# Kernel optimization log

Hardware: AMD Instinct MI355X
Metric: run time of the kernel (lower is better)

## Reference

```python
import jax, jax.numpy as jnp
import numpy as np

B, N, M = 64, 256, 16
ONF, OEF = 92, 41
NF, EF = 128, 64
FINAL = 128  # final_node_len; final_layer outputs FINAL//2


def _linear_params(key, fan_in, fan_out):
    # kaiming_uniform fan_in, relu: bound = sqrt(6/fan_in)
    bound = np.sqrt(6.0 / fan_in)
    W = jax.random.uniform(key, (fan_out, fan_in), jnp.float32, -bound, bound)
    b = jnp.zeros((fan_out,), jnp.float32)
    return W, b


def setup_inputs() -> dict:
    key = jax.random.key(0)
    ks = jax.random.split(key, 12)
    node_fea = jax.random.normal(ks[0], (B, N, ONF), jnp.float32)
    edge_fea = jax.random.normal(ks[1], (B, N, M, OEF), jnp.float32)
    edge_fea_idx = jax.random.randint(ks[2], (B, N, M), 0, N)
    dis = jax.random.uniform(ks[3], (N, N), jnp.float32)
    Wn, bn = _linear_params(ks[4], ONF, NF)
    We, be = _linear_params(ks[5], OEF, EF)
    W1, b1 = _linear_params(ks[6], 2 * NF + EF, 2 * NF)
    W2, b2 = _linear_params(ks[7], 2 * NF + EF, 2 * NF)
    W3, b3 = _linear_params(ks[8], 2 * NF + EF, 2 * NF)
    Wf, bf = _linear_params(ks[9], NF, FINAL // 2)
    return dict(node_fea=node_fea, edge_fea=edge_fea, edge_fea_idx=edge_fea_idx,
                dis=dis, Wn=Wn, bn=bn, We=We, be=be,
                W1=W1, b1=b1, a1=jnp.float32(0.7),
                W2=W2, b2=b2, a2=jnp.float32(0.7),
                W3=W3, b3=b3, a3=jnp.float32(0.7),
                Wf=Wf, bf=bf,
                DAw=jnp.float32(48.0 / 5.0), DAb=jnp.float32(-28.0 / 5.0))


def _conv(nf, ef, idx, W, b, alpha):
    # nf: [B,N,F]; ef: [B,N,M,E]; idx: [B,N,M]
    Bb, Nn, Mm = idx.shape
    F = nf.shape[-1]
    idx_c = jnp.maximum(idx, 0)
    gathered = jax.vmap(lambda x, i: x[i])(nf, idx_c)           # [B,N,M,F]
    self_exp = jnp.broadcast_to(nf[:, :, None, :], (Bb, Nn, Mm, F))
    total = jnp.concatenate([self_exp, gathered, ef], axis=-1)   # [B,N,M,2F+E]
    gated = jnp.einsum('bnmi,oi->bnmo', total, W) + b            # [B,N,M,2F]
    nbr_filter, nbr_core = jnp.split(gated, 2, axis=-1)
    mask = (idx >= 0).astype(nf.dtype)[..., None]
    nbr_filter = jax.nn.sigmoid(nbr_filter) * mask
    nbr_core = jax.nn.softplus(nbr_core)
    nbr_sumed = jnp.sum(nbr_filter * nbr_core, axis=2)           # [B,N,F]
    return jax.nn.softplus(alpha * nf + nbr_sumed)


def reference(node_fea, edge_fea, edge_fea_idx, dis,
              Wn, bn, We, be,
              W1, b1, a1, W2, b2, a2, W3, b3, a3,
              Wf, bf, DAw, DAb):
    nf = node_fea @ Wn.T + bn                                    # [B,N,NF]
    ef = edge_fea @ We.T + be                                    # [B,N,M,EF]
    nf = _conv(nf, ef, edge_fea_idx, W1, b1, a1)
    nf = _conv(nf, ef, edge_fea_idx, W2, b2, a2)
    nf = _conv(nf, ef, edge_fea_idx, W3, b3, a3)
    nf = nf @ Wf.T + bf                                          # [B,N,FINAL//2]
    DA = jax.nn.sigmoid(DAw * dis + DAb)                         # [N,N]
    node1 = jnp.einsum('ij,bjf->bif', DA, nf)
    return jnp.concatenate([nf, node1], axis=2)                  # [B,N,FINAL]
```

## Files before the change

### kernel.cpp

```cpp
#include <hip/hip_runtime.h>
#include <hip/hip_bf16.h>
#include <math.h>

#define Bb   64
#define Nn   256
#define Mm   16
#define ONF  92
#define OEF  41
#define NF   128
#define EF   64
#define KDIM 320
#define ODIM 256
#define FINAL 128
#define K0C  6
#define GRP  4
#define NODESB (4*GRP)

#define LOG2E_F 1.44269504088896f
#define LN2_F   0.6931471805599453f

typedef __attribute__((ext_vector_type(8))) short short8;
typedef __attribute__((ext_vector_type(4))) float f32x4;

#define AS1 __attribute__((address_space(1)))
#define AS3 __attribute__((address_space(3)))

__device__ __forceinline__ void gl2lds16(const void* gp, void* lp) {
    __builtin_amdgcn_global_load_lds((AS1 void*)(void*)gp, (AS3 void*)lp, 16, 0, 0);
}
#define KEEP8(x) asm volatile("" : "+v"(x))

__device__ __forceinline__ float sigmoidf_(float x) {
    float e = __expf(-x);
    return __builtin_amdgcn_rcpf(1.0f + e);
}
__device__ __forceinline__ float softplusf_(float x) {
    return fmaxf(x, 0.0f) + __logf(1.0f + __expf(-fabsf(x)));
}
__device__ __forceinline__ __hip_bfloat16 to_bf16(float x) { return __float2bfloat16(x); }

__device__ __forceinline__ void swz(const float* __restrict__ in, __hip_bfloat16* __restrict__ out,
                                    int t, int Itot, int koff, int Kuse, int K0, float scale)
{
    int j = t & 7;
    int u = t >> 3;
    int lane = u & 63;
    int ln16 = lane & 15, q = lane >> 4;
    int v = u >> 6;
    int k0 = v % K0, tile = v / K0;
    int n = tile * 16 + ln16, k = k0 * 32 + q * 8 + j;
    out[t] = (k < Kuse) ? to_bf16(scale * in[(size_t)n * Itot + koff + k]) : to_bf16(0.0f);
}

#define SZ_WET (OEF * EF)
#define SZ_WB  (16 * K0C * 512)
#define SZ_WS  (16 * 4 * 512)
#define SZ_WNB ((NF / 16) * 3 * 512)
#define SZ_WEB ((EF / 16) * 2 * 512)
#define SZ_WFB ((64 / 16) * 4 * 512)
#define SZ_DA  (Nn * Nn)
#define PREP_TOTAL (SZ_WET + 3 * SZ_WB + 3 * SZ_WS + SZ_WNB + SZ_WEB + SZ_WFB + SZ_DA)

__global__ __launch_bounds__(256) void k_prep(
    const float* __restrict__ We, const float* __restrict__ W1,
    const float* __restrict__ W2, const float* __restrict__ W3,
    const float* __restrict__ Wn, const float* __restrict__ Wf,
    const float* __restrict__ dis, const float* __restrict__ pw, const float* __restrict__ pb,
    float* __restrict__ WeT,
    __hip_bfloat16* __restrict__ W1b, __hip_bfloat16* __restrict__ W2b, __hip_bfloat16* __restrict__ W3b,
    __hip_bfloat16* __restrict__ W1s, __hip_bfloat16* __restrict__ W2s, __hip_bfloat16* __restrict__ W3s,
    __hip_bfloat16* __restrict__ Wnb, __hip_bfloat16* __restrict__ Web, __hip_bfloat16* __restrict__ Wfb,
    __hip_bfloat16* __restrict__ DAf)
{
    int t = blockIdx.x * 256 + threadIdx.x;
    if (t < SZ_WET) {
        int o = t / OEF, i = t - o * OEF;
        WeT[i * EF + o] = We[t];
        return;
    }
    t -= SZ_WET;
    if (t < SZ_WB) { swz(W1, W1b, t, KDIM, NF, 192, K0C, LOG2E_F); return; }
    t -= SZ_WB;
    if (t < SZ_WB) { swz(W2, W2b, t, KDIM, NF, 192, K0C, LOG2E_F); return; }
    t -= SZ_WB;
    if (t < SZ_WB) { swz(W3, W3b, t, KDIM, NF, 192, K0C, LOG2E_F); return; }
    t -= SZ_WB;
    if (t < SZ_WS) { swz(W1, W1s, t, KDIM, 0, NF, 4, LOG2E_F); return; }
    t -= SZ_WS;
    if (t < SZ_WS) { swz(W2, W2s, t, KDIM, 0, NF, 4, LOG2E_F); return; }
    t -= SZ_WS;
    if (t < SZ_WS) { swz(W3, W3s, t, KDIM, 0, NF, 4, LOG2E_F); return; }
    t -= SZ_WS;
    if (t < SZ_WNB) { swz(Wn, Wnb, t, ONF, 0, ONF, 3, 1.0f); return; }
    t -= SZ_WNB;
    if (t < SZ_WEB) { swz(We, Web, t, OEF, 0, OEF, 2, 1.0f); return; }
    t -= SZ_WEB;
    if (t < SZ_WFB) { swz(Wf, Wfb, t, NF, 0, NF, 4, 1.0f); return; }
    t -= SZ_WFB;
    if (t < SZ_DA) {
        int i = t >> 8, jx = t & 255;
        float v = sigmoidf_(fmaf(*pw, dis[t], *pb));
        int itile = i >> 4, ln16 = i & 15;
        int k0 = jx >> 5, q = (jx >> 3) & 3, jj = jx & 7;
        DAf[(size_t)((((itile * 8 + k0) << 6) + (q << 4) + ln16)) * 8 + jj] = to_bf16(v);
    }
}

template<int KIN, int K0, int NCOLS>
__device__ __forceinline__ void emb_body(
    int bid, const float* __restrict__ X, const __hip_bfloat16* __restrict__ Bswz,
    const float* __restrict__ bias, __hip_bfloat16* __restrict__ Y,
    __hip_bfloat16* A_s, __hip_bfloat16* O_s)
{
    constexpr int KP = K0 * 32;
    constexpr int TPW = NCOLS / 64;
    constexpr int OLD = NCOLS + 24;

    const int row0 = bid * 64;
    const int t = threadIdx.x;

    {
        const float4* Xb = (const float4*)(X + (size_t)row0 * KIN);
        constexpr int NV = (64 * KIN) / 4;
        for (int c = t; c < NV; c += 256) {
            float4 v = Xb[c];
            int flat = c * 4;
            #pragma unroll
            for (int e = 0; e < 4; e++) {
                int f = flat + e;
                int row = f / KIN, k = f - row * KIN;
                int mt = row >> 4, ln16 = row & 15;
                int k0 = k >> 5, q = (k >> 3) & 3, j = k & 7;
                float vv = (e == 0) ? v.x : (e == 1) ? v.y : (e == 2) ? v.z : v.w;
                A_s[(((mt * K0 + k0) << 6) + (q << 4) + ln16) * 8 + j] = to_bf16(vv);
            }
        }
        constexpr int PAD = KP - KIN;
        for (int c = t; c < 64 * PAD; c += 256) {
            int row = c / PAD, k = KIN + (c - row * PAD);
            int mt = row >> 4, ln16 = row & 15;
            int k0 = k >> 5, q = (k >> 3) & 3, j = k & 7;
            A_s[(((mt * K0 + k0) << 6) + (q << 4) + ln16) * 8 + j] = to_bf16(0.0f);
        }
    }
    __syncthreads();

    const int wv = t >> 6, lane = t & 63;
    const int q = lane >> 4, ln16 = lane & 15;

    f32x4 acc[4][TPW];
    #pragma unroll
    for (int p = 0; p < TPW; p++) {
        float bv = bias[(wv * TPW + p) * 16 + ln16];
        #pragma unroll
        for (int mt = 0; mt < 4; mt++) acc[mt][p] = (f32x4){bv, bv, bv, bv};
    }

    short8 bw[TPW][K0];
    #pragma unroll
    for (int p = 0; p < TPW; p++)
        #pragma unroll
        for (int k0 = 0; k0 < K0; k0++)
            bw[p][k0] = *(const short8*)(Bswz + ((size_t)((wv * TPW + p) * K0 + k0) << 9) + (lane << 3));

    #pragma unroll
    for (int k0 = 0; k0 < K0; k0++) {
        short8 af[4];
        #pragma unroll
        for (int mt = 0; mt < 4; mt++)
            af[mt] = *(const short8*)(A_s + (((mt * K0 + k0) << 6) + lane) * 8);
        #pragma unroll
        for (int mt = 0; mt < 4; mt++)
            #pragma unroll
            for (int p = 0; p < TPW; p++)
                acc[mt][p] = __builtin_amdgcn_mfma_f32_16x16x32_bf16(af[mt], bw[p][k0], acc[mt][p], 0, 0, 0);
    }

    #pragma unroll
    for (int mt = 0; mt < 4; mt++)
        #pragma unroll
        for (int p = 0; p < TPW; p++) {
            int col = (wv * TPW + p) * 16 + ln16;
            #pragma unroll
            for (int r = 0; r < 4; r++)
                O_s[(mt * 16 + q * 4 + r) * OLD + col] = to_bf16(acc[mt][p][r]);
        }
    __syncthreads();
    constexpr int CH = NCOLS / 8;
    for (int c = t; c < 64 * CH; c += 256) {
        int row = c / CH, ch = c - row * CH;
        *(uint4*)(Y + (size_t)(row0 + row) * NCOLS + ch * 8) =
            *(const uint4*)(O_s + row * OLD + ch * 8);
    }
}

__global__ __launch_bounds__(256) void k_embed_all(
    const float* __restrict__ node_fea, const __hip_bfloat16* __restrict__ Wnb,
    const float* __restrict__ bn, __hip_bfloat16* __restrict__ nf0,
    const float* __restrict__ edge_fea, const __hip_bfloat16* __restrict__ Web,
    const float* __restrict__ be, __hip_bfloat16* __restrict__ efb)
{
    __shared__ __align__(16) __hip_bfloat16 A_s[4 * 3 * 512];
    __shared__ __align__(16) __hip_bfloat16 O_s[64 * (NF + 24)];
    if (blockIdx.x < 256)
        emb_body<ONF, 3, NF>(blockIdx.x, node_fea, Wnb, bn, nf0, A_s, O_s);
    else
        emb_body<OEF, 2, EF>(blockIdx.x - 256, edge_fea, Web, be, efb, A_s, O_s);
}

__global__ __launch_bounds__(256, 3) void k_conv_blk(
    const __hip_bfloat16* __restrict__ nf_in,
    const __hip_bfloat16* __restrict__ ef_bf,
    const int*   __restrict__ eidx,
    const __hip_bfloat16* __restrict__ Wb,
    const __hip_bfloat16* __restrict__ Wsb,
    const float* __restrict__ bias,
    const float* __restrict__ palpha,
    __hip_bfloat16* __restrict__ nf_out)
{
    __shared__ __align__(16) __hip_bfloat16 A_s[2][4 * K0C * 512];

    const int node0_blk = blockIdx.x * NODESB;
    const int bbase = node0_blk & ~255;
    const int t = threadIdx.x;
    const int wv = t >> 6, lane = t & 63;
    const int q = lane >> 4, ln16 = lane & 15;
    const int row = (wv << 4) + ln16;
    const float alpha = *palpha;

    auto stage_group = [&](int node0g, __hip_bfloat16* buf) -> unsigned long long {
        int mi = eidx[node0g * Mm + row];
        unsigned long long mb = __ballot(eidx[node0g * Mm + lane] >= 0);
        int j = mi < 0 ? 0 : mi;
        const __hip_bfloat16* gathp = nf_in + (size_t)(bbase + j) * NF + q * 8;
        #pragma unroll
        for (int k0 = 0; k0 < 4; k0++)
            gl2lds16(gathp + k0 * 32, buf + (wv * K0C + k0) * 512 + lane * 8);
        const __hip_bfloat16* efp = ef_bf + (size_t)((node0g << 4) + row) * EF + q * 8;
        #pragma unroll
        for (int k0 = 0; k0 < 2; k0++)
            gl2lds16(efp + k0 * 32, buf + (wv * K0C + 4 + k0) * 512 + lane * 8);
        return mb;
    };

    unsigned long long mb_next = stage_group(node0_blk, A_s[0]);

    const __hip_bfloat16* WF0 = Wb + ((size_t)(2 * wv) * (K0C * 512)) + (lane << 3);
    const __hip_bfloat16* WF1 = WF0 + K0C * 512;
    const __hip_bfloat16* WC0 = WF0 + 8 * (K0C * 512);
    const __hip_bfloat16* WC1 = WC0 + K0C * 512;
    short8 mF0[K0C], mF1[K0C], mC0[K0C], mC1[K0C];
    #pragma unroll
    for (int k0 = 0; k0 < K0C; k0++) {
        mF0[k0] = *(const short8*)(WF0 + k0 * 512);
        mF1[k0] = *(const short8*)(WF1 + k0 * 512);
        mC0[k0] = *(const short8*)(WC0 + k0 * 512);
        mC1[k0] = *(const short8*)(WC1 + k0 * 512);
    }

    f32x4 sv[4];
    #pragma unroll
    for (int c = 0; c < 4; c++) {
        int tile = 2 * wv + (c & 1) + ((c >> 1) << 3);
        float bv = bias[tile * 16 + ln16] * LOG2E_F;
        sv[c] = (f32x4){bv, bv, bv, bv};
    }
    #pragma unroll
    for (int k0 = 0; k0 < 4; k0++) {
        short8 afs = *(const short8*)(nf_in + (size_t)(node0_blk + ln16) * NF + k0 * 32 + q * 8);
        #pragma unroll
        for (int c = 0; c < 4; c++) {
            int tile = 2 * wv + (c & 1) + ((c >> 1) << 3);
            short8 bws = *(const short8*)(Wsb + ((size_t)(tile * 4 + k0) << 9) + (lane << 3));
            sv[c] = __builtin_amdgcn_mfma_f32_16x16x32_bf16(afs, bws, sv[c], 0, 0, 0);
        }
    }

    #pragma unroll
    for (int k0 = 0; k0 < K0C; k0++) {
        KEEP8(mF0[k0]); KEEP8(mF1[k0]); KEEP8(mC0[k0]); KEEP8(mC1[k0]);
    }

    __syncthreads();

    int cur = 0;
    for (int g = 0; g < GRP; g++) {
        const int node0g = node0_blk + g * 4;
        const unsigned long long mb_cur = mb_next;
        if (g + 1 < GRP) mb_next = stage_group(node0g + 4, A_s[cur ^ 1]);

        float selfv[8];
        #pragma unroll
        for (int mt = 0; mt < 4; mt++)
            #pragma unroll
            for (int p = 0; p < 2; p++)
                selfv[mt * 2 + p] =
                    __bfloat162float(nf_in[(size_t)(node0g + mt) * NF + (2 * wv + p) * 16 + ln16]);

        const int srcl = (g << 4) + ln16;
        const __hip_bfloat16* Acur = A_s[cur];

        #pragma unroll
        for (int h = 0; h < 2; h++) {
            f32x4 accF[2][2], accC[2][2];
            #pragma unroll
            for (int mtl = 0; mtl < 2; mtl++) {
                const int mt = 2 * h + mtl;
                #pragma unroll
                for (int p = 0; p < 2; p++) {
                    float vF = __shfl(sv[p][mt], srcl);
                    float vC = __shfl(sv[2 + p][mt], srcl);
                    accF[mtl][p] = (f32x4){vF, vF, vF, vF};
                    accC[mtl][p] = (f32x4){vC, vC, vC, vC};
                }
            }
            #pragma unroll
            for (int k0 = 0; k0 < K0C; k0++) {
                short8 af[2];
                #pragma unroll
                for (int mtl = 0; mtl < 2; mtl++)
                    af[mtl] = *(const short8*)(Acur + (((2 * h + mtl) * K0C + k0) * 64 + lane) * 8);
                #pragma unroll
                for (int mtl = 0; mtl < 2; mtl++) {
                    accF[mtl][0] = __builtin_amdgcn_mfma_f32_16x16x32_bf16(af[mtl], mF0[k0], accF[mtl][0], 0, 0, 0);
                    accF[mtl][1] = __builtin_amdgcn_mfma_f32_16x16x32_bf16(af[mtl], mF1[k0], accF[mtl][1], 0, 0, 0);
                    accC[mtl][0] = __builtin_amdgcn_mfma_f32_16x16x32_bf16(af[mtl], mC0[k0], accC[mtl][0], 0, 0, 0);
                    accC[mtl][1] = __builtin_amdgcn_mfma_f32_16x16x32_bf16(af[mtl], mC1[k0], accC[mtl][1], 0, 0, 0);
                }
            }
            #pragma unroll
            for (int mtl = 0; mtl < 2; mtl++) {
                const int mt = 2 * h + mtl;
                const int gnode = node0g + mt;
                unsigned mbits = (unsigned)(mb_cur >> (mt * 16 + q * 4)) & 0xFu;
                #pragma unroll
                for (int p = 0; p < 2; p++) {
                    float partial = 0.0f;
                    #pragma unroll
                    for (int r = 0; r < 4; r++) {
                        bool msk = (mbits >> r) & 1u;
                        float f2 = accF[mtl][p][r];
                        float c2 = accC[mtl][p][r];
                        float sig = __builtin_amdgcn_rcpf(1.0f + __builtin_amdgcn_exp2f(-f2));
                        float sp2 = fmaxf(c2, 0.0f) +
                                    __builtin_amdgcn_logf(1.0f + __builtin_amdgcn_exp2f(-fabsf(c2)));
                        partial += msk ? sig * sp2 : 0.0f;
                    }
                    partial += __shfl_xor(partial, 16);
                    partial += __shfl_xor(partial, 32);
                    if (q == 0) {
                        int col = (2 * wv + p) * 16 + ln16;
                        nf_out[(size_t)gnode * NF + col] =
                            to_bf16(softplusf_(fmaf(alpha, selfv[mt * 2 + p], LN2_F * partial)));
                    }
                }
            }
        }
        __syncthreads();
        cur ^= 1;
    }
}

template<bool PRECOMP>
__global__ __launch_bounds__(256, 3) void k_conv_mfma(
    const __hip_bfloat16* __restrict__ nf_in,
    const float* __restrict__ edge_fea,
    const __hip_bfloat16* __restrict__ ef_bf,
    const int*   __restrict__ eidx,
    const float* __restrict__ WeT,
    const float* __restrict__ be,
    const __hip_bfloat16* __restrict__ Wb,
    const __hip_bfloat16* __restrict__ Wsb,
    const float* __restrict__ bias,
    const float* __restrict__ palpha,
    __hip_bfloat16* __restrict__ nf_out)
{
    __shared__ __align__(16) __hip_bfloat16 A_s[4 * K0C * 512];
    __shared__ __align__(16) __hip_bfloat16 A_sf[4 * 512];

    const int node0 = blockIdx.x * 4;
    const int b = node0 >> 8;
    const int t = threadIdx.x;
    const int wv = t >> 6, lane = t & 63;
    const int q = lane >> 4, ln16 = lane & 15;
    const int row = (wv << 4) + ln16;

    const int myidx = eidx[node0 * Mm + row];
    const unsigned long long mball = __ballot(eidx[node0 * Mm + lane] >= 0);

    float selfv[8];
    #pragma unroll
    for (int mt = 0; mt < 4; mt++)
        #pragma unroll
        for (int p = 0; p < 2; p++)
            selfv[mt * 2 + p] =
                __bfloat162float(nf_in[(size_t)(node0 + mt) * NF + (2 * wv + p) * 16 + ln16]);

    {
        int j = myidx < 0 ? 0 : myidx;
        const __hip_bfloat16* gathp = nf_in + (size_t)((b << 8) + j) * NF;
        #pragma unroll
        for (int k0 = 0; k0 < 4; k0++)
            *(uint4*)(A_s + ((wv * K0C + k0) * 64 + lane) * 8) =
                *(const uint4*)(gathp + k0 * 32 + q * 8);
        *(uint4*)(A_sf + (wv * 64 + lane) * 8) =
            *(const uint4*)(nf_in + (size_t)(node0 + (ln16 & 3)) * NF + wv * 32 + q * 8);
        if (PRECOMP) {
            const __hip_bfloat16* efp = ef_bf + (size_t)((node0 << 4) + row) * EF;
            #pragma unroll
            for (int k0 = 0; k0 < 2; k0++)
                *(uint4*)(A_s + ((wv * K0C + 4 + k0) * 64 + lane) * 8) =
                    *(const uint4*)(efp + k0 * 32 + q * 8);
        } else {
            for (int c = t; c < 64 * EF; c += 256) {
                int rr = c >> 6, col = c & 63;
                float a = be[col];
                const float* er = edge_fea + (size_t)(node0 * Mm + rr) * OEF;
                #pragma unroll
                for (int i = 0; i < OEF; i++) a = fmaf(er[i], WeT[i * EF + col], a);
                int mt = rr >> 4, l16 = rr & 15;
                int k0 = 4 + (col >> 5), qq = (col >> 3) & 3, jj = col & 7;
                A_s[((mt * K0C + k0) * 64 + qq * 16 + l16) * 8 + jj] = to_bf16(a);
            }
        }
    }
    __syncthreads();

    f32x4 sv[4];
    #pragma unroll
    for (int c = 0; c < 4; c++) {
        int tile = 2 * wv + (c & 1) + ((c >> 1) << 3);
        float bv = bias[tile * 16 + ln16] * LOG2E_F;
        sv[c] = (f32x4){bv, bv, bv, bv};
    }
    #pragma unroll
    for (int k0 = 0; k0 < 4; k0++) {
        short8 afs = *(const short8*)(A_sf + (k0 * 64 + lane) * 8);
        #pragma unroll
        for (int c = 0; c < 4; c++) {
            int tile = 2 * wv + (c & 1) + ((c >> 1) << 3);
            short8 bws = *(const short8*)(Wsb + ((size_t)(tile * 4 + k0) << 9) + (lane << 3));
            sv[c] = __builtin_amdgcn_mfma_f32_16x16x32_bf16(afs, bws, sv[c], 0, 0, 0);
        }
    }

    f32x4 accF[4][2], accC[4][2];
    #pragma unroll
    for (int mt = 0; mt < 4; mt++) {
        #pragma unroll
        for (int p = 0; p < 2; p++) {
            float vF = __shfl(sv[p][mt], ln16);
            float vC = __shfl(sv[2 + p][mt], ln16);
            accF[mt][p] = (f32x4){vF, vF, vF, vF};
            accC[mt][p] = (f32x4){vC, vC, vC, vC};
        }
    }

    const __hip_bfloat16* WF0 = Wb + ((size_t)(2 * wv) * (K0C * 512)) + (lane << 3);
    const __hip_bfloat16* WF1 = WF0 + K0C * 512;
    const __hip_bfloat16* WC0 = WF0 + 8 * (K0C * 512);
    const __hip_bfloat16* WC1 = WC0 + K0C * 512;

    #pragma unroll
    for (int k0 = 0; k0 < K0C; k0++) {
        short8 cF0 = *(const short8*)(WF0 + k0 * 512);
        short8 cF1 = *(const short8*)(WF1 + k0 * 512);
        short8 cC0 = *(const short8*)(WC0 + k0 * 512);
        short8 cC1 = *(const short8*)(WC1 + k0 * 512);
        short8 af[4];
        #pragma unroll
        for (int mt = 0; mt < 4; mt++)
            af[mt] = *(const short8*)(A_s + ((mt * K0C + k0) * 64 + lane) * 8);
        #pragma unroll
        for (int mt = 0; mt < 4; mt++) {
            accF[mt][0] = __builtin_amdgcn_mfma_f32_16x16x32_bf16(af[mt], cF0, accF[mt][0], 0, 0, 0);
            accF[mt][1] = __builtin_amdgcn_mfma_f32_16x16x32_bf16(af[mt], cF1, accF[mt][1], 0, 0, 0);
            accC[mt][0] = __builtin_amdgcn_mfma_f32_16x16x32_bf16(af[mt], cC0, accC[mt][0], 0, 0, 0);
            accC[mt][1] = __builtin_amdgcn_mfma_f32_16x16x32_bf16(af[mt], cC1, accC[mt][1], 0, 0, 0);
        }
    }

    const float alpha = *palpha;
    #pragma unroll
    for (int mt = 0; mt < 4; mt++) {
        const int gnode = node0 + mt;
        unsigned mbits = (unsigned)(mball >> (mt * 16 + q * 4)) & 0xFu;
        #pragma unroll
        for (int p = 0; p < 2; p++) {
            float partial = 0.0f;
            #pragma unroll
            for (int r = 0; r < 4; r++) {
                bool msk = (mbits >> r) & 1u;
                float f2 = accF[mt][p][r];
                float c2 = accC[mt][p][r];
                float sig = __builtin_amdgcn_rcpf(1.0f + __builtin_amdgcn_exp2f(-f2));
                float sp2 = fmaxf(c2, 0.0f) +
                            __builtin_amdgcn_logf(1.0f + __builtin_amdgcn_exp2f(-fabsf(c2)));
                partial += msk ? sig * sp2 : 0.0f;
            }
            partial += __shfl_xor(partial, 16);
            partial += __shfl_xor(partial, 32);
            if (q == 0) {
                int col = (2 * wv + p) * 16 + ln16;
                nf_out[(size_t)gnode * NF + col] =
                    to_bf16(softplusf_(fmaf(alpha, selfv[mt * 2 + p], LN2_F * partial)));
            }
        }
    }
}

__global__ __launch_bounds__(256) void k_final_mfma(
    const __hip_bfloat16* __restrict__ nf, const __hip_bfloat16* __restrict__ Wfb,
    const float* __restrict__ bfv, float* __restrict__ out,
    __hip_bfloat16* __restrict__ XT)
{
    __shared__ __align__(16) __hip_bfloat16 A_s[16 * 512];
    const int node0 = blockIdx.x * 64;
    const int bloc = node0 >> 8;
    const int t = threadIdx.x;
    const int wv = t >> 6, lane = t & 63;
    const int q = lane >> 4, ln16 = lane & 15;

    const __hip_bfloat16* rowp = nf + (size_t)(node0 + (wv << 4) + ln16) * NF;
    #pragma unroll
    for (int k0 = 0; k0 < 4; k0++)
        *(uint4*)(A_s + ((wv * 4 + k0) * 64 + lane) * 8) =
            *(const uint4*)(rowp + k0 * 32 + q * 8);
    __syncthreads();

    short8 bw[4];
    #pragma unroll
    for (int k0 = 0; k0 < 4; k0++)
        bw[k0] = *(const short8*)(Wfb + ((size_t)(wv * 4 + k0) * 64 + lane) * 8);

    float bv = bfv[wv * 16 + ln16];
    f32x4 acc[4];
    #pragma unroll
    for (int mt = 0; mt < 4; mt++) acc[mt] = (f32x4){bv, bv, bv, bv};

    #pragma unroll
    for (int k0 = 0; k0 < 4; k0++) {
        short8 af[4];
        #pragma unroll
        for (int mt = 0; mt < 4; mt++)
            af[mt] = *(const short8*)(A_s + ((mt * 4 + k0) * 64 + lane) * 8);
        #pragma unroll
        for (int mt = 0; mt < 4; mt++)
            acc[mt] = __builtin_amdgcn_mfma_f32_16x16x32_bf16(af[mt], bw[k0], acc[mt], 0, 0, 0);
    }

    const int col = (wv << 4) + ln16;
    #pragma unroll
    for (int mt = 0; mt < 4; mt++)
        #pragma unroll
        for (int r = 0; r < 4; r++) {
            int row = mt * 16 + q * 4 + r;
            float v = acc[mt][r];
            out[(size_t)(node0 + row) * FINAL + col] = v;
            XT[(size_t)(bloc * 64 + col) * 256 + (node0 & 255) + row] = to_bf16(v);
        }
}

__global__ __launch_bounds__(256) void k_node1_mfma(
    const __hip_bfloat16* __restrict__ DAf,
    const __hip_bfloat16* __restrict__ XT,
    float* __restrict__ out)
{
    __shared__ __align__(16) __hip_bfloat16 B_s[32 * 512];
    const int blk = blockIdx.x;
    const int b = blk >> 2, i0 = (blk & 3) * 64;
    const int t = threadIdx.x;
    const int wv = t >> 6, lane = t & 63;
    const int q = lane >> 4, ln16 = lane & 15;

    const __hip_bfloat16* xrow = XT + (size_t)(b * 64 + (wv << 4) + ln16) * 256;
    #pragma unroll
    for (int k0 = 0; k0 < 8; k0++)
        *(uint4*)(B_s + ((wv * 8 + k0) * 64 + lane) * 8) =
            *(const uint4*)(xrow + k0 * 32 + q * 8);
    __syncthreads();

    f32x4 acc[4];
    #pragma unroll
    for (int mt = 0; mt < 4; mt++) acc[mt] = (f32x4){0.f, 0.f, 0.f, 0.f};

    #pragma unroll
    for (int k0 = 0; k0 < 8; k0++) {
        short8 bfr = *(const short8*)(B_s + ((wv * 8 + k0) * 64 + lane) * 8);
        short8 af[4];
        #pragma unroll
        for (int mt = 0; mt < 4; mt++)
            af[mt] = *(const short8*)(DAf + (size_t)(((i0 >> 4) + mt) * 8 + k0) * 512 + (lane << 3));
        #pragma unroll
        for (int mt = 0; mt < 4; mt++)
            acc[mt] = __builtin_amdgcn_mfma_f32_16x16x32_bf16(af[mt], bfr, acc[mt], 0, 0, 0);
    }

    #pragma unroll
    for (int mt = 0; mt < 4; mt++)
        #pragma unroll
        for (int r = 0; r < 4; r++) {
            int i = i0 + mt * 16 + q * 4 + r;
            out[(size_t)((b << 8) + i) * FINAL + 64 + (wv << 4) + ln16] = acc[mt][r];
        }
}

extern "C" void kernel_launch(void* const* d_in, const int* in_sizes, int n_in,
                              void* d_out, int out_size, void* d_ws, size_t ws_size,
                              hipStream_t stream)
{
    const float* node_fea = (const float*)d_in[0];
    const float* edge_fea = (const float*)d_in[1];
    const int*   eidx     = (const int*)  d_in[2];
    const float* dis      = (const float*)d_in[3];
    const float* Wn = (const float*)d_in[4];
    const float* bn = (const float*)d_in[5];
    const float* We = (const float*)d_in[6];
    const float* be = (const float*)d_in[7];
    const float* W1 = (const float*)d_in[8];
    const float* b1 = (const float*)d_in[9];
    const float* a1 = (const float*)d_in[10];
    const float* W2 = (const float*)d_in[11];
    const float* b2 = (const float*)d_in[12];
    const float* a2 = (const float*)d_in[13];
    const float* W3 = (const float*)d_in[14];
    const float* b3 = (const float*)d_in[15];
    const float* a3 = (const float*)d_in[16];
    const float* Wf = (const float*)d_in[17];
    const float* bf = (const float*)d_in[18];
    const float* DAw = (const float*)d_in[19];
    const float* DAb = (const float*)d_in[20];
    float* out = (float*)d_out;

    char* base = (char*)d_ws;
    size_t off = 0;
    auto alloc = [&](size_t bytes) { char* p = base + off; off = (off + bytes + 255) & ~(size_t)255; return p; };
    __hip_bfloat16* nfA = (__hip_bfloat16*)alloc((size_t)Bb * Nn * NF * 2);
    __hip_bfloat16* nfB = (__hip_bfloat16*)alloc((size_t)Bb * Nn * NF * 2);
    __hip_bfloat16* W1b = (__hip_bfloat16*)alloc((size_t)SZ_WB * 2);
    __hip_bfloat16* W2b = (__hip_bfloat16*)alloc((size_t)SZ_WB * 2);
    __hip_bfloat16* W3b = (__hip_bfloat16*)alloc((size_t)SZ_WB * 2);
    __hip_bfloat16* W1s = (__hip_bfloat16*)alloc((size_t)SZ_WS * 2);
    __hip_bfloat16* W2s = (__hip_bfloat16*)alloc((size_t)SZ_WS * 2);
    __hip_bfloat16* W3s = (__hip_bfloat16*)alloc((size_t)SZ_WS * 2);
    float* WeT = (float*)alloc((size_t)OEF * EF * 4);
    __hip_bfloat16* DAf = (__hip_bfloat16*)alloc((size_t)Nn * Nn * 2);
    __hip_bfloat16* Wnb = (__hip_bfloat16*)alloc((size_t)SZ_WNB * 2);
    __hip_bfloat16* Web = (__hip_bfloat16*)alloc((size_t)SZ_WEB * 2);
    __hip_bfloat16* Wfb = (__hip_bfloat16*)alloc((size_t)SZ_WFB * 2);
    __hip_bfloat16* XT  = (__hip_bfloat16*)alloc((size_t)Bb * 64 * Nn * 2);
    __hip_bfloat16* efb = (__hip_bfloat16*)alloc((size_t)Bb * Nn * Mm * EF * 2);
    const bool precomp = (ws_size >= off);

    hipLaunchKernelGGL(k_prep, dim3((PREP_TOTAL + 255) / 256), dim3(256), 0, stream,
                       We, W1, W2, W3, Wn, Wf, dis, DAw, DAb,
                       WeT, W1b, W2b, W3b, W1s, W2s, W3s, Wnb, Web, Wfb, DAf);

    hipLaunchKernelGGL(k_embed_all, dim3(precomp ? (256 + Bb * Nn * Mm / 64) : 256), dim3(256), 0, stream,
                       node_fea, Wnb, bn, nfA, edge_fea, Web, be, efb);

    if (precomp) {
        hipLaunchKernelGGL(k_conv_blk, dim3(Bb * Nn / NODESB), dim3(256), 0, stream,
                           nfA, efb, eidx, W1b, W1s, b1, a1, nfB);
        hipLaunchKernelGGL(k_conv_blk, dim3(Bb * Nn / NODESB), dim3(256), 0, stream,
                           nfB, efb, eidx, W2b, W2s, b2, a2, nfA);
        hipLaunchKernelGGL(k_conv_blk, dim3(Bb * Nn / NODESB), dim3(256), 0, stream,
                           nfA, efb, eidx, W3b, W3s, b3, a3, nfB);
    } else {
        hipLaunchKernelGGL((k_conv_mfma<false>), dim3(Bb * Nn / 4), dim3(256), 0, stream,
                           nfA, edge_fea, efb, eidx, WeT, be, W1b, W1s, b1, a1, nfB);
        hipLaunchKernelGGL((k_conv_mfma<false>), dim3(Bb * Nn / 4), dim3(256), 0, stream,
                           nfB, edge_fea, efb, eidx, WeT, be, W2b, W2s, b2, a2, nfA);
        hipLaunchKernelGGL((k_conv_mfma<false>), dim3(Bb * Nn / 4), dim3(256), 0, stream,
                           nfA, edge_fea, efb, eidx, WeT, be, W3b, W3s, b3, a3, nfB);
    }

    hipLaunchKernelGGL(k_final_mfma, dim3(Bb * Nn / 64), dim3(256), 0, stream, nfB, Wfb, bf, out, XT);
    hipLaunchKernelGGL(k_node1_mfma, dim3(Bb * 4), dim3(256), 0, stream, DAf, XT, out);
}
```

Before: 316.8 us.

## Split self-term GEMM into separate kernel and make conv kernel persistent

The per-node self-feature projection (nf times the self slice of W plus bias) moves out of the conv kernel into a standalone MFMA GEMM kernel that writes a float32 S buffer. The conv kernel becomes persistent with a fixed grid of 768 blocks, grid-striding over 4-node groups with double-buffered LDS staging of neighbour and edge tiles. It reads the precomputed S row for each node. This amortises the register-resident weight loads across more groups and removes the per-block self-GEMM and shuffles. In exchange it adds three extra launches and a 16 MB float32 round trip through memory per layer.

```diff
diff --git a/kernel.cpp b/kernel.cpp
--- a/kernel.cpp
+++ b/kernel.cpp
@@ -13,8 +13,8 @@
 #define ODIM 256
 #define FINAL 128
 #define K0C  6
-#define GRP  4
-#define NODESB (4*GRP)
+#define NGRP  (Bb * Nn / 4)
+#define GRIDP 768
 
 #define LOG2E_F 1.44269504088896f
 #define LN2_F   0.6931471805599453f
@@ -208,27 +208,83 @@
         emb_body<OEF, 2, EF>(blockIdx.x - 256, edge_fea, Web, be, efb, A_s, O_s);
 }
 
-__global__ __launch_bounds__(256, 3) void k_conv_blk(
+__global__ __launch_bounds__(256) void k_gemm_s(
+    const __hip_bfloat16* __restrict__ nf,
+    const __hip_bfloat16* __restrict__ Ws,
+    const float* __restrict__ bias,
+    float* __restrict__ S)
+{
+    __shared__ __align__(16) __hip_bfloat16 A_s[16 * 512];
+    const int row0 = blockIdx.x * 64;
+    const int t = threadIdx.x;
+    const int wv = t >> 6, lane = t & 63;
+    const int q = lane >> 4, ln16 = lane & 15;
+
+    #pragma unroll
+    for (int k0 = 0; k0 < 4; k0++)
+        gl2lds16(nf + (size_t)(row0 + (wv << 4) + ln16) * NF + k0 * 32 + q * 8,
+                 A_s + ((wv * 4 + k0) * 64 + lane) * 8);
+    __syncthreads();
+
+    short8 bw[4][4];
+    #pragma unroll
+    for (int p = 0; p < 4; p++)
+        #pragma unroll
+        for (int k0 = 0; k0 < 4; k0++)
+            bw[p][k0] = *(const short8*)(Ws + ((size_t)((wv * 4 + p) * 4 + k0) << 9) + (lane << 3));
+
+    f32x4 acc[4][4];
+    #pragma unroll
+    for (int p = 0; p < 4; p++) {
+        float bv = bias[(wv * 4 + p) * 16 + ln16] * LOG2E_F;
+        #pragma unroll
+        for (int mt = 0; mt < 4; mt++) acc[mt][p] = (f32x4){bv, bv, bv, bv};
+    }
+
+    #pragma unroll
+    for (int k0 = 0; k0 < 4; k0++) {
+        short8 af[4];
+        #pragma unroll
+        for (int mt = 0; mt < 4; mt++)
+            af[mt] = *(const short8*)(A_s + ((mt * 4 + k0) * 64 + lane) * 8);
+        #pragma unroll
+        for (int mt = 0; mt < 4; mt++)
+            #pragma unroll
+            for (int p = 0; p < 4; p++)
+                acc[mt][p] = __builtin_amdgcn_mfma_f32_16x16x32_bf16(af[mt], bw[p][k0], acc[mt][p], 0, 0, 0);
+    }
+
+    #pragma unroll
+    for (int mt = 0; mt < 4; mt++)
+        #pragma unroll
+        for (int p = 0; p < 4; p++) {
+            int col = (wv * 4 + p) * 16 + ln16;
+            #pragma unroll
+            for (int r = 0; r < 4; r++)
+                S[(size_t)(row0 + mt * 16 + q * 4 + r) * ODIM + col] = acc[mt][p][r];
+        }
+}
+
+__global__ __launch_bounds__(256, 3) void k_conv_ps(
     const __hip_bfloat16* __restrict__ nf_in,
     const __hip_bfloat16* __restrict__ ef_bf,
     const int*   __restrict__ eidx,
     const __hip_bfloat16* __restrict__ Wb,
-    const __hip_bfloat16* __restrict__ Wsb,
-    const float* __restrict__ bias,
+    const float* __restrict__ Sbuf,
     const float* __restrict__ palpha,
     __hip_bfloat16* __restrict__ nf_out)
 {
     __shared__ __align__(16) __hip_bfloat16 A_s[2][4 * K0C * 512];
 
-    const int node0_blk = blockIdx.x * NODESB;
-    const int bbase = node0_blk & ~255;
     const int t = threadIdx.x;
     const int wv = t >> 6, lane = t & 63;
     const int q = lane >> 4, ln16 = lane & 15;
     const int row = (wv << 4) + ln16;
     const float alpha = *palpha;
 
-    auto stage_group = [&](int node0g, __hip_bfloat16* buf) -> unsigned long long {
+    auto stage_group = [&](int gi, __hip_bfloat16* buf) -> unsigned long long {
+        const int node0g = gi * 4;
+        const int bbase = node0g & ~255;
         int mi = eidx[node0g * Mm + row];
         unsigned long long mb = __ballot(eidx[node0g * Mm + lane] >= 0);
         int j = mi < 0 ? 0 : mi;
@@ -242,8 +298,6 @@
             gl2lds16(efp + k0 * 32, buf + (wv * K0C + 4 + k0) * 512 + lane * 8);
         return mb;
     };
-
-    unsigned long long mb_next = stage_group(node0_blk, A_s[0]);
 
     const __hip_bfloat16* WF0 = Wb + ((size_t)(2 * wv) * (K0C * 512)) + (lane << 3);
     const __hip_bfloat16* WF1 = WF0 + K0C * 512;
@@ -258,105 +312,70 @@
         mC1[k0] = *(const short8*)(WC1 + k0 * 512);
     }
 
-    f32x4 sv[4];
-    #pragma unroll
-    for (int c = 0; c < 4; c++) {
-        int tile = 2 * wv + (c & 1) + ((c >> 1) << 3);
-        float bv = bias[tile * 16 + ln16] * LOG2E_F;
-        sv[c] = (f32x4){bv, bv, bv, bv};
-    }
-    #pragma unroll
-    for (int k0 = 0; k0 < 4; k0++) {
-        short8 afs = *(const short8*)(nf_in + (size_t)(node0_blk + ln16) * NF + k0 * 32 + q * 8);
-        #pragma unroll
-        for (int c = 0; c < 4; c++) {
-            int tile = 2 * wv + (c & 1) + ((c >> 1) << 3);
-            short8 bws = *(const short8*)(Wsb + ((size_t)(tile * 4 + k0) << 9) + (lane << 3));
-            sv[c] = __builtin_amdgcn_mfma_f32_16x16x32_bf16(afs, bws, sv[c], 0, 0, 0);
-        }
-    }
-
-    #pragma unroll
-    for (int k0 = 0; k0 < K0C; k0++) {
-        KEEP8(mF0[k0]); KEEP8(mF1[k0]); KEEP8(mC0[k0]); KEEP8(mC1[k0]);
-    }
-
-    __syncthreads();
-
+    int g = blockIdx.x;
+    unsigned long long mb_pending = stage_group(g, A_s[0]);
     int cur = 0;
-    for (int g = 0; g < GRP; g++) {
-        const int node0g = node0_blk + g * 4;
-        const unsigned long long mb_cur = mb_next;
-        if (g + 1 < GRP) mb_next = stage_group(node0g + 4, A_s[cur ^ 1]);
-
-        float selfv[8];
-        #pragma unroll
-        for (int mt = 0; mt < 4; mt++)
-            #pragma unroll
-            for (int p = 0; p < 2; p++)
-                selfv[mt * 2 + p] =
-                    __bfloat162float(nf_in[(size_t)(node0g + mt) * NF + (2 * wv + p) * 16 + ln16]);
-
-        const int srcl = (g << 4) + ln16;
+
+    for (; g < NGRP; g += GRIDP) {
+        __syncthreads();
+
+        const unsigned long long mb_now = mb_pending;
+        if (g + GRIDP < NGRP) mb_pending = stage_group(g + GRIDP, A_s[cur ^ 1]);
+
+        #pragma unroll
+        for (int k0 = 0; k0 < K0C; k0++) {
+            KEEP8(mF0[k0]); KEEP8(mF1[k0]); KEEP8(mC0[k0]); KEEP8(mC1[k0]);
+        }
+
+        const int node0g = g * 4;
         const __hip_bfloat16* Acur = A_s[cur];
 
         #pragma unroll
-        for (int h = 0; h < 2; h++) {
-            f32x4 accF[2][2], accC[2][2];
-            #pragma unroll
-            for (int mtl = 0; mtl < 2; mtl++) {
-                const int mt = 2 * h + mtl;
+        for (int mt = 0; mt < 4; mt++) {
+            const int gnode = node0g + mt;
+            const float* Srow = Sbuf + (size_t)gnode * ODIM;
+            f32x4 accF[2], accC[2];
+            float selfv[2];
+            #pragma unroll
+            for (int p = 0; p < 2; p++) {
+                int col = (2 * wv + p) * 16 + ln16;
+                float vF = Srow[col];
+                float vC = Srow[128 + col];
+                accF[p] = (f32x4){vF, vF, vF, vF};
+                accC[p] = (f32x4){vC, vC, vC, vC};
+                selfv[p] = __bfloat162float(nf_in[(size_t)gnode * NF + col]);
+            }
+            #pragma unroll
+            for (int k0 = 0; k0 < K0C; k0++) {
+                short8 af = *(const short8*)(Acur + ((mt * K0C + k0) * 64 + lane) * 8);
+                accF[0] = __builtin_amdgcn_mfma_f32_16x16x32_bf16(af, mF0[k0], accF[0], 0, 0, 0);
+                accF[1] = __builtin_amdgcn_mfma_f32_16x16x32_bf16(af, mF1[k0], accF[1], 0, 0, 0);
+                accC[0] = __builtin_amdgcn_mfma_f32_16x16x32_bf16(af, mC0[k0], accC[0], 0, 0, 0);
+                accC[1] = __builtin_amdgcn_mfma_f32_16x16x32_bf16(af, mC1[k0], accC[1], 0, 0, 0);
+            }
+            unsigned mbits = (unsigned)(mb_now >> (mt * 16 + q * 4)) & 0xFu;
+            #pragma unroll
+            for (int p = 0; p < 2; p++) {
+                float partial = 0.0f;
                 #pragma unroll
-                for (int p = 0; p < 2; p++) {
-                    float vF = __shfl(sv[p][mt], srcl);
-                    float vC = __shfl(sv[2 + p][mt], srcl);
-                    accF[mtl][p] = (f32x4){vF, vF, vF, vF};
-                    accC[mtl][p] = (f32x4){vC, vC, vC, vC};
+                for (int r = 0; r < 4; r++) {
+                    bool msk = (mbits >> r) & 1u;
+                    float f2 = accF[p][r];
+                    float c2 = accC[p][r];
+                    float sig = __builtin_amdgcn_rcpf(1.0f + __builtin_amdgcn_exp2f(-f2));
+                    float sp2 = fmaxf(c2, 0.0f) +
+                                __builtin_amdgcn_logf(1.0f + __builtin_amdgcn_exp2f(-fabsf(c2)));
+                    partial += msk ? sig * sp2 : 0.0f;
+                }
+                partial += __shfl_xor(partial, 16);
+                partial += __shfl_xor(partial, 32);
+                if (q == 0) {
+                    int col = (2 * wv + p) * 16 + ln16;
+                    nf_out[(size_t)gnode * NF + col] =
+                        to_bf16(softplusf_(fmaf(alpha, selfv[p], LN2_F * partial)));
                 }
             }
-            #pragma unroll
-            for (int k0 = 0; k0 < K0C; k0++) {
-                short8 af[2];
-                #pragma unroll
-                for (int mtl = 0; mtl < 2; mtl++)
-                    af[mtl] = *(const short8*)(Acur + (((2 * h + mtl) * K0C + k0) * 64 + lane) * 8);
-                #pragma unroll
-                for (int mtl = 0; mtl < 2; mtl++) {
-                    accF[mtl][0] = __builtin_amdgcn_mfma_f32_16x16x32_bf16(af[mtl], mF0[k0], accF[mtl][0], 0, 0, 0);
-                    accF[mtl][1] = __builtin_amdgcn_mfma_f32_16x16x32_bf16(af[mtl], mF1[k0], accF[mtl][1], 0, 0, 0);
-                    accC[mtl][0] = __builtin_amdgcn_mfma_f32_16x16x32_bf16(af[mtl], mC0[k0], accC[mtl][0], 0, 0, 0);
-                    accC[mtl][1] = __builtin_amdgcn_mfma_f32_16x16x32_bf16(af[mtl], mC1[k0], accC[mtl][1], 0, 0, 0);
-                }
-            }
-            #pragma unroll
-            for (int mtl = 0; mtl < 2; mtl++) {
-                const int mt = 2 * h + mtl;
-                const int gnode = node0g + mt;
-                unsigned mbits = (unsigned)(mb_cur >> (mt * 16 + q * 4)) & 0xFu;
-                #pragma unroll
-                for (int p = 0; p < 2; p++) {
-                    float partial = 0.0f;
-                    #pragma unroll
-                    for (int r = 0; r < 4; r++) {
-                        bool msk = (mbits >> r) & 1u;
-                        float f2 = accF[mtl][p][r];
-                        float c2 = accC[mtl][p][r];
-                        float sig = __builtin_amdgcn_rcpf(1.0f + __builtin_amdgcn_exp2f(-f2));
-                        float sp2 = fmaxf(c2, 0.0f) +
-                                    __builtin_amdgcn_logf(1.0f + __builtin_amdgcn_exp2f(-fabsf(c2)));
-                        partial += msk ? sig * sp2 : 0.0f;
-                    }
-                    partial += __shfl_xor(partial, 16);
-                    partial += __shfl_xor(partial, 32);
-                    if (q == 0) {
-                        int col = (2 * wv + p) * 16 + ln16;
-                        nf_out[(size_t)gnode * NF + col] =
-                            to_bf16(softplusf_(fmaf(alpha, selfv[mt * 2 + p], LN2_F * partial)));
-                    }
-                }
-            }
-        }
-        __syncthreads();
+        }
         cur ^= 1;
     }
 }
@@ -650,6 +669,7 @@
     __hip_bfloat16* Wfb = (__hip_bfloat16*)alloc((size_t)SZ_WFB * 2);
     __hip_bfloat16* XT  = (__hip_bfloat16*)alloc((size_t)Bb * 64 * Nn * 2);
     __hip_bfloat16* efb = (__hip_bfloat16*)alloc((size_t)Bb * Nn * Mm * EF * 2);
+    float* Sbuf = (float*)alloc((size_t)Bb * Nn * ODIM * 4);
     const bool precomp = (ws_size >= off);
 
     hipLaunchKernelGGL(k_prep, dim3((PREP_TOTAL + 255) / 256), dim3(256), 0, stream,
@@ -660,12 +680,18 @@
                        node_fea, Wnb, bn, nfA, edge_fea, Web, be, efb);
 
     if (precomp) {
-        hipLaunchKernelGGL(k_conv_blk, dim3(Bb * Nn / NODESB), dim3(256), 0, stream,
-                           nfA, efb, eidx, W1b, W1s, b1, a1, nfB);
-        hipLaunchKernelGGL(k_conv_blk, dim3(Bb * Nn / NODESB), dim3(256), 0, stream,
-                           nfB, efb, eidx, W2b, W2s, b2, a2, nfA);
-        hipLaunchKernelGGL(k_conv_blk, dim3(Bb * Nn / NODESB), dim3(256), 0, stream,
-                           nfA, efb, eidx, W3b, W3s, b3, a3, nfB);
+        hipLaunchKernelGGL(k_gemm_s, dim3(Bb * Nn / 64), dim3(256), 0, stream,
+                           nfA, W1s, b1, Sbuf);
+        hipLaunchKernelGGL(k_conv_ps, dim3(GRIDP), dim3(256), 0, stream,
+                           nfA, efb, eidx, W1b, Sbuf, a1, nfB);
+        hipLaunchKernelGGL(k_gemm_s, dim3(Bb * Nn / 64), dim3(256), 0, stream,
+                           nfB, W2s, b2, Sbuf);
+        hipLaunchKernelGGL(k_conv_ps, dim3(GRIDP), dim3(256), 0, stream,
+                           nfB, efb, eidx, W2b, Sbuf, a2, nfA);
+        hipLaunchKernelGGL(k_gemm_s, dim3(Bb * Nn / 64), dim3(256), 0, stream,
+                           nfA, W3s, b3, Sbuf);
+        hipLaunchKernelGGL(k_conv_ps, dim3(GRIDP), dim3(256), 0, stream,
+                           nfA, efb, eidx, W3b, Sbuf, a3, nfB);
     } else {
         hipLaunchKernelGGL((k_conv_mfma<false>), dim3(Bb * Nn / 4), dim3(256), 0, stream,
                            nfA, edge_fea, efb, eidx, WeT, be, W1b, W1s, b1, a1, nfB);
```

After: 313.1 us. Within noise of the previous version (-1.2%).
